# Kernel tuning notes

Hardware: AMD Instinct MI355X
Metric: run time of the kernel (lower is better)

The kernel has to match this reference:

```python
import jax, jax.numpy as jnp
import numpy as np

N = 20000        # nodes
E = 320000       # edges (avg degree 16)
F_IN = 256       # n_feat
HID = 64         # n_hid (per-head channels, layer 1)
HEADS = 8        # hard-coded n_head in GAT2
NCLS = 64        # n_classes
NEG_SLOPE = 0.2  # PyG GATv2Conv default leaky_relu slope
EPS = 1e-16      # PyG softmax denominator epsilon


def setup_inputs() -> dict:
    key = jax.random.key(0)
    ks = jax.random.split(key, 10)
    glorot = lambda k, shape: jax.random.normal(k, shape, jnp.float32) * (1.0 / np.sqrt(shape[0]))
    return {
        "x": jax.random.normal(ks[0], (N, F_IN), jnp.float32),
        "edge_index": jax.random.randint(ks[1], (2, E), 0, N, dtype=jnp.int32),
        # layer 1: GATv2Conv(F_IN -> HID, heads=HEADS, concat=True)
        "Wl1": glorot(ks[2], (F_IN, HEADS * HID)),
        "Wr1": glorot(ks[3], (F_IN, HEADS * HID)),
        "att1": glorot(ks[4], (HEADS, HID)),
        "b1": jnp.zeros((HEADS * HID,), jnp.float32),
        # layer 2: GATv2Conv(HEADS*HID -> NCLS, heads=1, concat=False)
        "Wl2": glorot(ks[5], (HEADS * HID, NCLS)),
        "Wr2": glorot(ks[6], (HEADS * HID, NCLS)),
        "att2": glorot(ks[7], (1, NCLS)),
        "b2": jnp.zeros((NCLS,), jnp.float32),
    }


def gatv2_layer(x, Wl, Wr, att, bias, src, dst, heads, concat):
    # x: [N, Fin]; Wl/Wr: [Fin, heads*C]; att: [heads, C]
    n = x.shape[0]
    c = att.shape[1]
    xl = (x @ Wl).reshape(n, heads, c)   # source-side projection
    xr = (x @ Wr).reshape(n, heads, c)   # target-side projection
    # per-edge GATv2 score: a^T leaky_relu(Wl x_j + Wr x_i)
    e = jax.nn.leaky_relu(xl[src] + xr[dst], NEG_SLOPE)      # [E, H, C]
    alpha = jnp.einsum('ehc,hc->eh', e, att)                 # [E, H]
    # segment softmax over incoming edges of each target node
    amax = jax.ops.segment_max(alpha, dst, num_segments=n)   # [N, H]
    amax = jnp.where(jnp.isfinite(amax), amax, 0.0)
    ex = jnp.exp(alpha - amax[dst])
    denom = jax.ops.segment_sum(ex, dst, num_segments=n)     # [N, H]
    w = ex / (denom[dst] + EPS)                              # [E, H]
    # weighted scatter-aggregate of source features
    out = jax.ops.segment_sum(xl[src] * w[:, :, None], dst, num_segments=n)  # [N, H, C]
    out = out.reshape(n, heads * c) if concat else out.mean(axis=1)
    return out + bias


def reference(x, edge_index, Wl1, Wr1, att1, b1, Wl2, Wr2, att2, b2):
    src, dst = edge_index[0], edge_index[1]
    h = gatv2_layer(x, Wl1, Wr1, att1, b1, src, dst, HEADS, True)   # [N, 512]
    h = jax.nn.elu(h)
    out = gatv2_layer(h, Wl2, Wr2, att2, b2, src, dst, 1, False)    # [N, 64]
    return out
```

## Files before the change

### kernel.cpp

```cpp
#include <hip/hip_runtime.h>
#include <hip/hip_bf16.h>

#define N_NODES 20000
#define N_EDGES 320000
#define F_IN 256
#define HID 64
#define HEADS 8
#define NCLS 64
#define D1 (HEADS * HID)
#define SCAN_BLOCKS ((N_NODES + 255) / 256)

typedef __attribute__((ext_vector_type(8))) short short8;
typedef __attribute__((ext_vector_type(4))) float floatx4;
typedef __attribute__((ext_vector_type(2))) float v2f;

__device__ __forceinline__ ushort f2bf(float f) {
    unsigned u = __float_as_uint(f);
    unsigned r = (u + 0x7fffu + ((u >> 16) & 1u)) >> 16;
    return (ushort)r;
}
__device__ __forceinline__ v2f unpack2(unsigned u) {
    v2f r;
    r.x = __uint_as_float(u << 16);
    r.y = __uint_as_float(u & 0xffff0000u);
    return r;
}
template <int CTRL>
__device__ __forceinline__ float dppadd(float x) {
    int y = __builtin_amdgcn_update_dpp(0, __float_as_int(x), CTRL, 0xF, 0xF, true);
    return x + __int_as_float(y);
}
__device__ __forceinline__ float rowsum8(float x) {
    x = dppadd<0xB1>(x);
    x = dppadd<0x4E>(x);
    x = dppadd<0x141>(x);
    return x;
}
__device__ __forceinline__ float rowsum16(float x) {
    x = dppadd<0xB1>(x);
    x = dppadd<0x4E>(x);
    x = dppadd<0x124>(x);
    x = dppadd<0x128>(x);
    return x;
}
__device__ __forceinline__ void async_copy16(ushort* lds, const ushort* g) {
    __builtin_amdgcn_global_load_lds(
        (const __attribute__((address_space(1))) void*)g,
        (__attribute__((address_space(3))) void*)lds, 16, 0, 0);
}

#define PB_HIST 1250
#define PB_CONV 5000
#define PB_T1   512
#define PB_T2   128
#define PB_TOTAL (PB_HIST + PB_CONV + 2 * PB_T1 + 2 * PB_T2)
__global__ __launch_bounds__(256) void preprocess(
    const float* __restrict__ x, ushort* __restrict__ xbf,
    const float* __restrict__ Wl1, const float* __restrict__ Wr1,
    const float* __restrict__ Wl2, const float* __restrict__ Wr2,
    ushort* __restrict__ wt1, ushort* __restrict__ wt2,
    const int* __restrict__ dst, int* __restrict__ cnt) {
    int b = blockIdx.x, t = threadIdx.x;
    if (b < PB_HIST) {
        int i = b * 256 + t;
        if (i < N_EDGES) atomicAdd(&cnt[dst[i]], 1);
    } else if (b < PB_HIST + PB_CONV) {
        int i = (b - PB_HIST) * 256 + t;
        if (i < N_NODES * F_IN / 4) {
            float4 v = ((const float4*)x)[i];
            ushort4 o;
            o.x = f2bf(v.x); o.y = f2bf(v.y); o.z = f2bf(v.z); o.w = f2bf(v.w);
            ((ushort4*)xbf)[i] = o;
        }
    } else if (b < PB_HIST + PB_CONV + 2 * PB_T1) {
        int lb = b - PB_HIST - PB_CONV;
        const float* W = (lb < PB_T1) ? Wl1 : Wr1;
        ushort* Wt = wt1 + ((lb < PB_T1) ? 0 : D1 * F_IN);
        int i = (lb % PB_T1) * 256 + t;
        if (i < D1 * F_IN) {
            int n = i >> 8, k = i & 255;
            Wt[i] = f2bf(W[(size_t)k * D1 + n]);
        }
    } else {
        int lb = b - PB_HIST - PB_CONV - 2 * PB_T1;
        const float* W = (lb < PB_T2) ? Wl2 : Wr2;
        ushort* Wt = wt2 + ((lb < PB_T2) ? 0 : NCLS * D1);
        int i = (lb % PB_T2) * 256 + t;
        if (i < NCLS * D1) {
            int n = i >> 9, k = i & 511;
            Wt[i] = f2bf(W[(size_t)k * NCLS + n]);
        }
    }
}

__global__ __launch_bounds__(256) void scan_local(const int* __restrict__ cnt,
                                                  int* __restrict__ pscan,
                                                  int* __restrict__ bsum, int n) {
    int tid = threadIdx.x;
    int i = blockIdx.x * 256 + tid;
    int lane = tid & 63, wave = tid >> 6;
    int v = (i < n) ? cnt[i] : 0;
    int x = v;
    #pragma unroll
    for (int d = 1; d < 64; d <<= 1) {
        int y = __shfl_up(x, d);
        if (lane >= d) x += y;
    }
    __shared__ int wsum[4];
    if (lane == 63) wsum[wave] = x;
    __syncthreads();
    int woff = 0;
    for (int w2 = 0; w2 < wave; w2++) woff += wsum[w2];
    int incl = x + woff;
    if (i < n) pscan[i] = incl;
    if (tid == 255) bsum[blockIdx.x] = incl;
}

__global__ __launch_bounds__(256) void scan_finalize(const int* __restrict__ cnt,
                                                     const int* __restrict__ pscan,
                                                     const int* __restrict__ bsum,
                                                     int* __restrict__ row_ptr,
                                                     int* __restrict__ cursor, int n) {
    int t = threadIdx.x;
    int lane = t & 63, wave = t >> 6;
    int v = (t < SCAN_BLOCKS && t < blockIdx.x) ? bsum[t] : 0;
    #pragma unroll
    for (int mask = 1; mask < 64; mask <<= 1) v += __shfl_xor(v, mask);
    __shared__ int ws[4];
    __shared__ int soff;
    if (lane == 0) ws[wave] = v;
    __syncthreads();
    if (t == 0) soff = ws[0] + ws[1] + ws[2] + ws[3];
    __syncthreads();
    int i = blockIdx.x * 256 + t;
    if (i < n) {
        int incl = pscan[i] + soff;
        row_ptr[i + 1] = incl;
        cursor[i] = incl - cnt[i];
    }
    if (i == 0) row_ptr[0] = 0;
}

#define G1_NT 8
#define G1_MT ((N_NODES + 127) / 128)
#define G1_BLOCKS (G1_NT * G1_MT)
#define SC_BLOCKS (N_EDGES / 256)
__global__ __launch_bounds__(256) void gemm1_scatter(
    const ushort* __restrict__ A, const ushort* __restrict__ Bt,
    ushort* __restrict__ C,
    const int* __restrict__ src, const int* __restrict__ dst,
    int* __restrict__ cursor, int* __restrict__ csr_src) {
    if (blockIdx.x >= G1_BLOCKS) {
        int i = (blockIdx.x - G1_BLOCKS) * 256 + threadIdx.x;
        if (i < N_EDGES) {
            int d = dst[i];
            int pos = atomicAdd(&cursor[d], 1);
            csr_src[pos] = src[i];
        }
        return;
    }
    const int M = N_NODES, N = 2 * D1, K = F_IN;
    __shared__ ushort As[128 * 32];
    __shared__ ushort Bs[128 * 32];
    int tid = threadIdx.x;
    int rowBase = (blockIdx.x >> 3) * 128, colBase = (blockIdx.x & 7) * 128;
    int wave = tid >> 6, lane = tid & 63;
    int quad = lane >> 4, m16 = lane & 15;
    int rh = wave >> 1, chf = wave & 1;
    floatx4 acc[4][4];
    #pragma unroll
    for (int i = 0; i < 4; i++)
        #pragma unroll
        for (int j = 0; j < 4; j++) acc[i][j] = (floatx4){0.f, 0.f, 0.f, 0.f};

    for (int k0 = 0; k0 < K; k0 += 32) {
        #pragma unroll
        for (int i = 0; i < 2; i++) {
            int idx = i * 256 + tid;
            int r = idx >> 2, kq = (idx & 3) * 8;
            int grow = min(rowBase + r, M - 1);
            async_copy16(&As[idx * 8], A + (size_t)grow * K + k0 + kq);
            async_copy16(&Bs[idx * 8], Bt + (size_t)(colBase + r) * K + k0 + kq);
        }
        __syncthreads();
        short8 af[4], bfr[4];
        #pragma unroll
        for (int i = 0; i < 4; i++)
            af[i] = *(short8*)&As[(rh * 64 + i * 16 + m16) * 32 + quad * 8];
        #pragma unroll
        for (int j = 0; j < 4; j++)
            bfr[j] = *(short8*)&Bs[(chf * 64 + j * 16 + m16) * 32 + quad * 8];
        #pragma unroll
        for (int i = 0; i < 4; i++)
            #pragma unroll
            for (int j = 0; j < 4; j++)
                acc[i][j] = __builtin_amdgcn_mfma_f32_16x16x32_bf16(af[i], bfr[j], acc[i][j], 0, 0, 0);
        __syncthreads();
    }
    #pragma unroll
    for (int i = 0; i < 4; i++)
        #pragma unroll
        for (int j = 0; j < 4; j++)
            #pragma unroll
            for (int r = 0; r < 4; r++) {
                int row = rowBase + rh * 64 + i * 16 + quad * 4 + r;
                if (row < M) C[(size_t)row * N + colBase + chf * 64 + j * 16 + m16] = f2bf(acc[i][j][r]);
            }
}

__global__ __launch_bounds__(256) void gemm2_32x128(
    const ushort* __restrict__ A, const ushort* __restrict__ Bt,
    ushort* __restrict__ C) {
    const int K = D1;
    __shared__ ushort As[32 * 32];
    __shared__ ushort Bs[128 * 32];
    int tid = threadIdx.x;
    int rowBase = blockIdx.x * 32;
    int wave = tid >> 6, lane = tid & 63;
    int quad = lane >> 4, m16 = lane & 15;
    floatx4 acc[2][2];
    #pragma unroll
    for (int i = 0; i < 2; i++)
        #pragma unroll
        for (int j = 0; j < 2; j++) acc[i][j] = (floatx4){0.f, 0.f, 0.f, 0.f};

    for (int k0 = 0; k0 < K; k0 += 32) {
        if (tid < 128) {
            int r = tid >> 2, kq = (tid & 3) * 8;
            async_copy16(&As[tid * 8], A + (size_t)(rowBase + r) * K + k0 + kq);
        }
        #pragma unroll
        for (int i = 0; i < 2; i++) {
            int idx = i * 256 + tid;
            int r = idx >> 2, kq = (idx & 3) * 8;
            async_copy16(&Bs[idx * 8], Bt + (size_t)r * K + k0 + kq);
        }
        __syncthreads();
        short8 af[2], bfr[2];
        #pragma unroll
        for (int i = 0; i < 2; i++)
            af[i] = *(short8*)&As[(i * 16 + m16) * 32 + quad * 8];
        #pragma unroll
        for (int j = 0; j < 2; j++)
            bfr[j] = *(short8*)&Bs[(wave * 32 + j * 16 + m16) * 32 + quad * 8];
        #pragma unroll
        for (int i = 0; i < 2; i++)
            #pragma unroll
            for (int j = 0; j < 2; j++)
                acc[i][j] = __builtin_amdgcn_mfma_f32_16x16x32_bf16(af[i], bfr[j], acc[i][j], 0, 0, 0);
        __syncthreads();
    }
    #pragma unroll
    for (int i = 0; i < 2; i++)
        #pragma unroll
        for (int j = 0; j < 2; j++)
            #pragma unroll
            for (int r = 0; r < 4; r++) {
                int row = rowBase + i * 16 + quad * 4 + r;
                C[(size_t)row * 128 + wave * 32 + j * 16 + m16] = f2bf(acc[i][j][r]);
            }
}

#define L1PROC(cu, valid)                                                     \
    {                                                                         \
        v2f _c01 = unpack2((cu).x), _c23 = unpack2((cu).y);                   \
        v2f _c45 = unpack2((cu).z), _c67 = unpack2((cu).w);                   \
        v2f _v01 = _c01 + xr01, _v23 = _c23 + xr23;                           \
        v2f _v45 = _c45 + xr45, _v67 = _c67 + xr67;                           \
        v2f _sp = a6_01 * _v01 + a4_01 * __builtin_elementwise_abs(_v01);     \
        _sp = _sp + a6_23 * _v23 + a4_23 * __builtin_elementwise_abs(_v23);   \
        _sp = _sp + a6_45 * _v45 + a4_45 * __builtin_elementwise_abs(_v45);   \
        _sp = _sp + a6_67 * _v67 + a4_67 * __builtin_elementwise_abs(_v67);   \
        float _sc = _sp.x + _sp.y;                                            \
        _sc = rowsum8(_sc);                                                   \
        float _e = (valid) ? exp2f(_sc) : 0.f;                                \
        den += _e;                                                            \
        v2f _ev = {_e, _e};                                                   \
        ac01 = ac01 + _ev * _c01; ac23 = ac23 + _ev * _c23;                   \
        ac45 = ac45 + _ev * _c45; ac67 = ac67 + _ev * _c67;                   \
    }

__global__ __launch_bounds__(256) void attn_l1_fused(
    const ushort* __restrict__ xlr, const float* __restrict__ att,
    const float* __restrict__ b1,
    const int* __restrict__ row_ptr, const int* __restrict__ csr_src,
    ushort* __restrict__ h1out) {
    int wave = threadIdx.x >> 6, lane = threadIdx.x & 63;
    int d = blockIdx.x * 4 + wave;
    int start = row_ptr[d], deg = row_ptr[d + 1] - start;

    uint4 xru = *(const uint4*)(xlr + (size_t)d * 1024 + 512 + 8 * lane);
    v2f xr01 = unpack2(xru.x), xr23 = unpack2(xru.y);
    v2f xr45 = unpack2(xru.z), xr67 = unpack2(xru.w);
    const float C6 = 0.6f * 1.44269504f, C4 = 0.4f * 1.44269504f;
    float4 atA = *(const float4*)(att + 8 * lane);
    float4 atB = *(const float4*)(att + 8 * lane + 4);
    v2f a6_01 = {C6 * atA.x, C6 * atA.y}, a4_01 = {C4 * atA.x, C4 * atA.y};
    v2f a6_23 = {C6 * atA.z, C6 * atA.w}, a4_23 = {C4 * atA.z, C4 * atA.w};
    v2f a6_45 = {C6 * atB.x, C6 * atB.y}, a4_45 = {C4 * atB.x, C4 * atB.y};
    v2f a6_67 = {C6 * atB.z, C6 * atB.w}, a4_67 = {C4 * atB.z, C4 * atB.w};

    float den = 0.f;
    v2f ac01 = {0.f, 0.f}, ac23 = {0.f, 0.f}, ac45 = {0.f, 0.f}, ac67 = {0.f, 0.f};

    if (deg > 0) {
        const int* cs = csr_src + start;
        uint4 q0 = *(const uint4*)(xlr + (size_t)cs[0] * 1024 + 8 * lane);
        uint4 q1 = *(const uint4*)(xlr + (size_t)cs[min(1, deg - 1)] * 1024 + 8 * lane);
        uint4 q2 = *(const uint4*)(xlr + (size_t)cs[min(2, deg - 1)] * 1024 + 8 * lane);
        uint4 q3 = *(const uint4*)(xlr + (size_t)cs[min(3, deg - 1)] * 1024 + 8 * lane);
        for (int i0 = 0; i0 < deg; i0 += 4) {
            uint4 e0 = q0, e1 = q1, e2 = q2, e3 = q3;
            if (i0 + 4 < deg) q0 = *(const uint4*)(xlr + (size_t)cs[i0 + 4] * 1024 + 8 * lane);
            if (i0 + 5 < deg) q1 = *(const uint4*)(xlr + (size_t)cs[i0 + 5] * 1024 + 8 * lane);
            if (i0 + 6 < deg) q2 = *(const uint4*)(xlr + (size_t)cs[i0 + 6] * 1024 + 8 * lane);
            if (i0 + 7 < deg) q3 = *(const uint4*)(xlr + (size_t)cs[i0 + 7] * 1024 + 8 * lane);
            L1PROC(e0, true)
            L1PROC(e1, i0 + 1 < deg)
            L1PROC(e2, i0 + 2 < deg)
            L1PROC(e3, i0 + 3 < deg)
        }
    }
    float inv = 1.f / (den + 1e-16f);
    float4 bA = *(const float4*)(b1 + 8 * lane);
    float4 bB = *(const float4*)(b1 + 8 * lane + 4);
    float o0 = ac01.x * inv + bA.x;
    float o1 = ac01.y * inv + bA.y;
    float o2 = ac23.x * inv + bA.z;
    float o3 = ac23.y * inv + bA.w;
    float o4 = ac45.x * inv + bB.x;
    float o5 = ac45.y * inv + bB.y;
    float o6 = ac67.x * inv + bB.z;
    float o7 = ac67.y * inv + bB.w;
    o0 = o0 > 0.f ? o0 : (__expf(o0) - 1.f);
    o1 = o1 > 0.f ? o1 : (__expf(o1) - 1.f);
    o2 = o2 > 0.f ? o2 : (__expf(o2) - 1.f);
    o3 = o3 > 0.f ? o3 : (__expf(o3) - 1.f);
    o4 = o4 > 0.f ? o4 : (__expf(o4) - 1.f);
    o5 = o5 > 0.f ? o5 : (__expf(o5) - 1.f);
    o6 = o6 > 0.f ? o6 : (__expf(o6) - 1.f);
    o7 = o7 > 0.f ? o7 : (__expf(o7) - 1.f);
    ushort4 h0, h1v;
    h0.x = f2bf(o0); h0.y = f2bf(o1); h0.z = f2bf(o2); h0.w = f2bf(o3);
    h1v.x = f2bf(o4); h1v.y = f2bf(o5); h1v.z = f2bf(o6); h1v.w = f2bf(o7);
    *(ushort4*)(h1out + (size_t)d * D1 + 8 * lane) = h0;
    *(ushort4*)(h1out + (size_t)d * D1 + 8 * lane + 4) = h1v;
}

#define L2PROC(cu, valid)                                                     \
    {                                                                         \
        v2f _c01 = unpack2((cu).x), _c23 = unpack2((cu).y);                   \
        v2f _v01 = _c01 + yr01, _v23 = _c23 + yr23;                           \
        v2f _sp = at6_01 * _v01 + at4_01 * __builtin_elementwise_abs(_v01)    \
                + at6_23 * _v23 + at4_23 * __builtin_elementwise_abs(_v23);   \
        float _sc = _sp.x + _sp.y;                                            \
        _sc = rowsum16(_sc);                                                  \
        float _e = (valid) ? exp2f(_sc) : 0.f;                                \
        den += _e;                                                            \
        v2f _ev = {_e, _e};                                                   \
        ac01 = ac01 + _ev * _c01; ac23 = ac23 + _ev * _c23;                   \
    }

__device__ __forceinline__ float xgroup_sum(float x) {
    float t = __int_as_float(__builtin_amdgcn_ds_swizzle(__float_as_int(x), 0x401F));
    x += t;
    x += __shfl_xor(x, 32);
    return x;
}

__global__ __launch_bounds__(256) void attn_l2_fused(
    const ushort* __restrict__ ylr, const float* __restrict__ att2,
    const float* __restrict__ b2,
    const int* __restrict__ row_ptr, const int* __restrict__ csr_src,
    float* __restrict__ out) {
    int wave = threadIdx.x >> 6, lane = threadIdx.x & 63;
    int d = blockIdx.x * 4 + wave;
    int grp = lane >> 4, l15 = lane & 15;
    int start = row_ptr[d], deg = row_ptr[d + 1] - start;

    uint2 yru = *(const uint2*)(ylr + (size_t)d * 128 + 64 + 4 * l15);
    v2f yr01 = unpack2(yru.x), yr23 = unpack2(yru.y);
    float4 a2 = *(const float4*)(att2 + 4 * l15);
    const float C6 = 0.6f * 1.44269504f, C4 = 0.4f * 1.44269504f;
    v2f at6_01 = {C6 * a2.x, C6 * a2.y}, at4_01 = {C4 * a2.x, C4 * a2.y};
    v2f at6_23 = {C6 * a2.z, C6 * a2.w}, at4_23 = {C4 * a2.z, C4 * a2.w};

    float den = 0.f;
    v2f ac01 = {0.f, 0.f}, ac23 = {0.f, 0.f};

    if (deg > 0) {
        int S = (deg + 3) >> 2;
        const int* cs = csr_src + start;
        uint2 q0 = *(const uint2*)(ylr + (size_t)cs[min(grp, deg - 1)] * 128 + 4 * l15);
        uint2 q1 = *(const uint2*)(ylr + (size_t)cs[min(min(1, S - 1) * 4 + grp, deg - 1)] * 128 + 4 * l15);
        for (int i = 0; i < S; i++) {
            uint2 cu = q0;
            q0 = q1;
            if (i + 2 < S) {
                int p = min((i + 2) * 4 + grp, deg - 1);
                q1 = *(const uint2*)(ylr + (size_t)cs[p] * 128 + 4 * l15);
            }
            L2PROC(cu, 4 * i + grp < deg)
        }
        den = xgroup_sum(den);
        ac01.x = xgroup_sum(ac01.x);
        ac01.y = xgroup_sum(ac01.y);
        ac23.x = xgroup_sum(ac23.x);
        ac23.y = xgroup_sum(ac23.y);
    }
    if (grp == 0) {
        float inv = 1.f / (den + 1e-16f);
        float4 bv = *(const float4*)(b2 + 4 * l15);
        float4 o;
        o.x = ac01.x * inv + bv.x;
        o.y = ac01.y * inv + bv.y;
        o.z = ac23.x * inv + bv.z;
        o.w = ac23.y * inv + bv.w;
        *(float4*)(out + (size_t)d * NCLS + 4 * l15) = o;
    }
}

extern "C" void kernel_launch(void* const* d_in, const int* in_sizes, int n_in,
                              void* d_out, int out_size, void* d_ws, size_t ws_size,
                              hipStream_t stream) {
    const float* x    = (const float*)d_in[0];
    const int*   edge = (const int*)d_in[1];
    const float* Wl1  = (const float*)d_in[2];
    const float* Wr1  = (const float*)d_in[3];
    const float* att1 = (const float*)d_in[4];
    const float* b1   = (const float*)d_in[5];
    const float* Wl2  = (const float*)d_in[6];
    const float* Wr2  = (const float*)d_in[7];
    const float* att2 = (const float*)d_in[8];
    const float* b2   = (const float*)d_in[9];
    float* out = (float*)d_out;

    const int* srcv = edge;
    const int* dstv = edge + N_EDGES;

    ushort* xbf  = (ushort*)d_ws;
    ushort* wt1  = xbf + (size_t)N_NODES * F_IN;
    ushort* wt2  = wt1 + 2 * D1 * F_IN;
    ushort* xlr  = wt2 + 2 * NCLS * D1;
    ushort* h1   = xlr + (size_t)N_NODES * 2 * D1;
    ushort* ylr  = h1 + (size_t)N_NODES * D1;
    int* cnt     = (int*)(ylr + (size_t)N_NODES * 2 * NCLS);
    int* pscan   = cnt + N_NODES;
    int* bsum    = pscan + N_NODES;
    int* row_ptr = bsum + 128;
    int* cursor  = row_ptr + N_NODES + 1;
    int* csr_src = cursor + N_NODES;

    hipMemsetAsync(cnt, 0, N_NODES * sizeof(int), stream);
    preprocess<<<PB_TOTAL, 256, 0, stream>>>(x, xbf, Wl1, Wr1, Wl2, Wr2, wt1, wt2, dstv, cnt);
    scan_local<<<SCAN_BLOCKS, 256, 0, stream>>>(cnt, pscan, bsum, N_NODES);
    scan_finalize<<<SCAN_BLOCKS, 256, 0, stream>>>(cnt, pscan, bsum, row_ptr, cursor, N_NODES);
    gemm1_scatter<<<G1_BLOCKS + SC_BLOCKS, 256, 0, stream>>>(
        xbf, wt1, xlr, srcv, dstv, cursor, csr_src);
    attn_l1_fused<<<N_NODES / 4, 256, 0, stream>>>(xlr, att1, b1, row_ptr, csr_src, h1);
    gemm2_32x128<<<N_NODES / 32, 256, 0, stream>>>(h1, wt2, ylr);
    attn_l2_fused<<<N_NODES / 4, 256, 0, stream>>>(ylr, att2, b2, row_ptr, csr_src, out);
}
```

Measured before the change: 223.3 us.

## Split layer-1 attention across two waves per node with 4 channels per lane

The layer-1 attention kernel now gives each destination node a 128-thread block (two waves) instead of one wave, so each lane handles 4 channels rather than 8. The per-head dot product now reduces over 16 lanes instead of 8. The aim is more parallelism and more loads in flight for the gather-bound aggregation, with fewer registers per lane. In exchange each lane issues narrower 8-byte loads, the per-edge index reads and softmax exponentials are repeated across both waves, and there are 4x as many blocks.

```diff
diff --git a/kernel.cpp b/kernel.cpp
--- a/kernel.cpp
+++ b/kernel.cpp
@@ -29,12 +29,6 @@
 __device__ __forceinline__ float dppadd(float x) {
     int y = __builtin_amdgcn_update_dpp(0, __float_as_int(x), CTRL, 0xF, 0xF, true);
     return x + __int_as_float(y);
-}
-__device__ __forceinline__ float rowsum8(float x) {
-    x = dppadd<0xB1>(x);
-    x = dppadd<0x4E>(x);
-    x = dppadd<0x141>(x);
-    return x;
 }
 __device__ __forceinline__ float rowsum16(float x) {
     x = dppadd<0xB1>(x);
@@ -264,57 +258,47 @@
 #define L1PROC(cu, valid)                                                     \
     {                                                                         \
         v2f _c01 = unpack2((cu).x), _c23 = unpack2((cu).y);                   \
-        v2f _c45 = unpack2((cu).z), _c67 = unpack2((cu).w);                   \
         v2f _v01 = _c01 + xr01, _v23 = _c23 + xr23;                           \
-        v2f _v45 = _c45 + xr45, _v67 = _c67 + xr67;                           \
-        v2f _sp = a6_01 * _v01 + a4_01 * __builtin_elementwise_abs(_v01);     \
-        _sp = _sp + a6_23 * _v23 + a4_23 * __builtin_elementwise_abs(_v23);   \
-        _sp = _sp + a6_45 * _v45 + a4_45 * __builtin_elementwise_abs(_v45);   \
-        _sp = _sp + a6_67 * _v67 + a4_67 * __builtin_elementwise_abs(_v67);   \
+        v2f _sp = a6_01 * _v01 + a4_01 * __builtin_elementwise_abs(_v01)      \
+                + a6_23 * _v23 + a4_23 * __builtin_elementwise_abs(_v23);     \
         float _sc = _sp.x + _sp.y;                                            \
-        _sc = rowsum8(_sc);                                                   \
+        _sc = rowsum16(_sc);                                                  \
         float _e = (valid) ? exp2f(_sc) : 0.f;                                \
         den += _e;                                                            \
         v2f _ev = {_e, _e};                                                   \
         ac01 = ac01 + _ev * _c01; ac23 = ac23 + _ev * _c23;                   \
-        ac45 = ac45 + _ev * _c45; ac67 = ac67 + _ev * _c67;                   \
-    }
-
-__global__ __launch_bounds__(256) void attn_l1_fused(
+    }
+
+__global__ __launch_bounds__(128) void attn_l1_fused(
     const ushort* __restrict__ xlr, const float* __restrict__ att,
     const float* __restrict__ b1,
     const int* __restrict__ row_ptr, const int* __restrict__ csr_src,
     ushort* __restrict__ h1out) {
-    int wave = threadIdx.x >> 6, lane = threadIdx.x & 63;
-    int d = blockIdx.x * 4 + wave;
+    int d = blockIdx.x, t = threadIdx.x;
     int start = row_ptr[d], deg = row_ptr[d + 1] - start;
 
-    uint4 xru = *(const uint4*)(xlr + (size_t)d * 1024 + 512 + 8 * lane);
+    uint2 xru = *(const uint2*)(xlr + (size_t)d * 1024 + 512 + 4 * t);
     v2f xr01 = unpack2(xru.x), xr23 = unpack2(xru.y);
-    v2f xr45 = unpack2(xru.z), xr67 = unpack2(xru.w);
     const float C6 = 0.6f * 1.44269504f, C4 = 0.4f * 1.44269504f;
-    float4 atA = *(const float4*)(att + 8 * lane);
-    float4 atB = *(const float4*)(att + 8 * lane + 4);
-    v2f a6_01 = {C6 * atA.x, C6 * atA.y}, a4_01 = {C4 * atA.x, C4 * atA.y};
-    v2f a6_23 = {C6 * atA.z, C6 * atA.w}, a4_23 = {C4 * atA.z, C4 * atA.w};
-    v2f a6_45 = {C6 * atB.x, C6 * atB.y}, a4_45 = {C4 * atB.x, C4 * atB.y};
-    v2f a6_67 = {C6 * atB.z, C6 * atB.w}, a4_67 = {C4 * atB.z, C4 * atB.w};
+    float4 atv = *(const float4*)(att + 4 * t);
+    v2f a6_01 = {C6 * atv.x, C6 * atv.y}, a4_01 = {C4 * atv.x, C4 * atv.y};
+    v2f a6_23 = {C6 * atv.z, C6 * atv.w}, a4_23 = {C4 * atv.z, C4 * atv.w};
 
     float den = 0.f;
-    v2f ac01 = {0.f, 0.f}, ac23 = {0.f, 0.f}, ac45 = {0.f, 0.f}, ac67 = {0.f, 0.f};
+    v2f ac01 = {0.f, 0.f}, ac23 = {0.f, 0.f};
 
     if (deg > 0) {
         const int* cs = csr_src + start;
-        uint4 q0 = *(const uint4*)(xlr + (size_t)cs[0] * 1024 + 8 * lane);
-        uint4 q1 = *(const uint4*)(xlr + (size_t)cs[min(1, deg - 1)] * 1024 + 8 * lane);
-        uint4 q2 = *(const uint4*)(xlr + (size_t)cs[min(2, deg - 1)] * 1024 + 8 * lane);
-        uint4 q3 = *(const uint4*)(xlr + (size_t)cs[min(3, deg - 1)] * 1024 + 8 * lane);
+        uint2 q0 = *(const uint2*)(xlr + (size_t)cs[0] * 1024 + 4 * t);
+        uint2 q1 = *(const uint2*)(xlr + (size_t)cs[min(1, deg - 1)] * 1024 + 4 * t);
+        uint2 q2 = *(const uint2*)(xlr + (size_t)cs[min(2, deg - 1)] * 1024 + 4 * t);
+        uint2 q3 = *(const uint2*)(xlr + (size_t)cs[min(3, deg - 1)] * 1024 + 4 * t);
         for (int i0 = 0; i0 < deg; i0 += 4) {
-            uint4 e0 = q0, e1 = q1, e2 = q2, e3 = q3;
-            if (i0 + 4 < deg) q0 = *(const uint4*)(xlr + (size_t)cs[i0 + 4] * 1024 + 8 * lane);
-            if (i0 + 5 < deg) q1 = *(const uint4*)(xlr + (size_t)cs[i0 + 5] * 1024 + 8 * lane);
-            if (i0 + 6 < deg) q2 = *(const uint4*)(xlr + (size_t)cs[i0 + 6] * 1024 + 8 * lane);
-            if (i0 + 7 < deg) q3 = *(const uint4*)(xlr + (size_t)cs[i0 + 7] * 1024 + 8 * lane);
+            uint2 e0 = q0, e1 = q1, e2 = q2, e3 = q3;
+            if (i0 + 4 < deg) q0 = *(const uint2*)(xlr + (size_t)cs[i0 + 4] * 1024 + 4 * t);
+            if (i0 + 5 < deg) q1 = *(const uint2*)(xlr + (size_t)cs[i0 + 5] * 1024 + 4 * t);
+            if (i0 + 6 < deg) q2 = *(const uint2*)(xlr + (size_t)cs[i0 + 6] * 1024 + 4 * t);
+            if (i0 + 7 < deg) q3 = *(const uint2*)(xlr + (size_t)cs[i0 + 7] * 1024 + 4 * t);
             L1PROC(e0, true)
             L1PROC(e1, i0 + 1 < deg)
             L1PROC(e2, i0 + 2 < deg)
@@ -322,29 +306,18 @@
         }
     }
     float inv = 1.f / (den + 1e-16f);
-    float4 bA = *(const float4*)(b1 + 8 * lane);
-    float4 bB = *(const float4*)(b1 + 8 * lane + 4);
-    float o0 = ac01.x * inv + bA.x;
-    float o1 = ac01.y * inv + bA.y;
-    float o2 = ac23.x * inv + bA.z;
-    float o3 = ac23.y * inv + bA.w;
-    float o4 = ac45.x * inv + bB.x;
-    float o5 = ac45.y * inv + bB.y;
-    float o6 = ac67.x * inv + bB.z;
-    float o7 = ac67.y * inv + bB.w;
+    float4 bv = *(const float4*)(b1 + 4 * t);
+    float o0 = ac01.x * inv + bv.x;
+    float o1 = ac01.y * inv + bv.y;
+    float o2 = ac23.x * inv + bv.z;
+    float o3 = ac23.y * inv + bv.w;
     o0 = o0 > 0.f ? o0 : (__expf(o0) - 1.f);
     o1 = o1 > 0.f ? o1 : (__expf(o1) - 1.f);
     o2 = o2 > 0.f ? o2 : (__expf(o2) - 1.f);
     o3 = o3 > 0.f ? o3 : (__expf(o3) - 1.f);
-    o4 = o4 > 0.f ? o4 : (__expf(o4) - 1.f);
-    o5 = o5 > 0.f ? o5 : (__expf(o5) - 1.f);
-    o6 = o6 > 0.f ? o6 : (__expf(o6) - 1.f);
-    o7 = o7 > 0.f ? o7 : (__expf(o7) - 1.f);
-    ushort4 h0, h1v;
-    h0.x = f2bf(o0); h0.y = f2bf(o1); h0.z = f2bf(o2); h0.w = f2bf(o3);
-    h1v.x = f2bf(o4); h1v.y = f2bf(o5); h1v.z = f2bf(o6); h1v.w = f2bf(o7);
-    *(ushort4*)(h1out + (size_t)d * D1 + 8 * lane) = h0;
-    *(ushort4*)(h1out + (size_t)d * D1 + 8 * lane + 4) = h1v;
+    ushort4 hv;
+    hv.x = f2bf(o0); hv.y = f2bf(o1); hv.z = f2bf(o2); hv.w = f2bf(o3);
+    *(ushort4*)(h1out + (size_t)d * D1 + 4 * t) = hv;
 }
 
 #define L2PROC(cu, valid)                                                     \
@@ -457,7 +430,7 @@
     scan_finalize<<<SCAN_BLOCKS, 256, 0, stream>>>(cnt, pscan, bsum, row_ptr, cursor, N_NODES);
     gemm1_scatter<<<G1_BLOCKS + SC_BLOCKS, 256, 0, stream>>>(
         xbf, wt1, xlr, srcv, dstv, cursor, csr_src);
-    attn_l1_fused<<<N_NODES / 4, 256, 0, stream>>>(xlr, att1, b1, row_ptr, csr_src, h1);
+    attn_l1_fused<<<N_NODES, 128, 0, stream>>>(xlr, att1, b1, row_ptr, csr_src, h1);
     gemm2_32x128<<<N_NODES / 32, 256, 0, stream>>>(h1, wt2, ylr);
     attn_l2_fused<<<N_NODES / 4, 256, 0, stream>>>(ylr, att2, b2, row_ptr, csr_src, out);
 }
```

Measured after the change: 213.2 us. 1.05x faster.
